# Optimization experiments

Measured on AMD Instinct MI355X. Metric: run time of the kernel, lower is better.

## Reference

```python
import jax, jax.numpy as jnp
import numpy as np

SPLINE_ORDER = 3
TOP_K = 2
NUM_EXPERTS = 8


def _gram_basis(x, beta_w):
    # x: (B, C, H, W) post-tanh. Returns (B, C*(S+1), H, W).
    P0 = jnp.ones_like(x)
    P1 = x
    ps = [P0, P1]
    for i in range(2, SPLINE_ORDER + 1):
        n, m = i - 1, i
        # beta(n, m) = (m+n)*(m-n)*n^2 / (m^2/(4n^2-1)) * beta_weights[n]
        beta = (m + n) * (m - n) * (n ** 2) * (4.0 * n ** 2 - 1.0) / (m ** 2) * beta_w[n]
        P2 = x * ps[-1] - beta * ps[-2]
        ps.append(P2)
    return jnp.concatenate(ps, axis=1)


def _expert(x, poly_w, beta_w):
    # tanh -> Gram polynomial basis -> SiLU -> conv2d (padding=1, stride=1)
    g = jax.nn.silu(_gram_basis(jnp.tanh(x), beta_w))
    return jax.lax.conv_general_dilated(
        g, poly_w[0], window_strides=(1, 1), padding=[(1, 1), (1, 1)],
        dimension_numbers=('NCHW', 'OIHW', 'NCHW'))


def _cv_squared(v):
    # torch.var is unbiased (ddof=1)
    return jnp.var(v, ddof=1) / (jnp.mean(v) ** 2 + 1e-10)


def reference(x, w_gate, poly_weights, beta_weights):
    B = x.shape[0]
    # gating input: global average pool -> (B, C)
    gate_x = jnp.mean(x, axis=(2, 3))
    probs = jax.nn.softmax(gate_x @ w_gate, axis=1)  # softmax BEFORE topk, as in source
    top_vals, top_idx = jax.lax.top_k(probs, TOP_K + 1)
    tk_vals = top_vals[:, :TOP_K]
    tk_idx = top_idx[:, :TOP_K]
    tk_gates = tk_vals / (jnp.sum(tk_vals, axis=1, keepdims=True) + 1e-6)
    gates = jnp.zeros_like(probs).at[jnp.arange(B)[:, None], tk_idx].set(tk_gates)
    importance = gates.sum(axis=0)
    load = jnp.sum(gates > 0, axis=0).astype(jnp.float32)  # eval-mode load
    loss = (_cv_squared(importance) + _cv_squared(load)) * 0.01
    # All experts share parameters (ModuleList([experts]*num_experts)), so
    # sum_e gates[b,e] * expert_e(x[b]) == gates.sum(1)[b] * expert(x[b]).
    y = _expert(x, poly_weights, beta_weights) * jnp.sum(gates, axis=1)[:, None, None, None]
    return y, loss


def setup_inputs() -> dict:
    key = jax.random.key(0)
    k1, k2, k3, k4 = jax.random.split(key, 4)
    x = jax.random.normal(k1, (16, 32, 192, 192), dtype=jnp.float32)
    w_gate = jax.random.normal(k2, (32, NUM_EXPERTS), dtype=jnp.float32) * 0.1
    poly_weights = jax.random.normal(k3, (1, 32, 32 * (SPLINE_ORDER + 1), 3, 3), dtype=jnp.float32) * 0.05
    beta_weights = jax.random.normal(k4, (SPLINE_ORDER + 1,), dtype=jnp.float32) * 0.01
    return {"x": x, "w_gate": w_gate, "poly_weights": poly_weights, "beta_weights": beta_weights}
```

## Files before the change

### kernel.cpp

```cpp
#include <hip/hip_runtime.h>

typedef unsigned short u16;
typedef unsigned int u32;
typedef __attribute__((ext_vector_type(8))) short bf16x8;
typedef __attribute__((ext_vector_type(4))) float f32x4;

static constexpr int B = 16, C = 32, H = 192, W = 192;
static constexpr int HW = H * W;
static constexpr int E = 8;
static constexpr int CO = 32;
static constexpr int NB = 96;
static constexpr long long NTOT = (long long)B * C * HW;
static constexpr float SILU1 = 0.7310585786300049f;

static constexpr size_t GP_OFF  = (size_t)NTOT * 2;
static constexpr size_t SCL_OFF = GP_OFF + (size_t)B * C * NB * 4;
static constexpr size_t SK_OFF  = SCL_OFF + 128;
static constexpr size_t SS_OFF  = SK_OFF + 288 * 4;
static constexpr size_t WF_OFF  = SS_OFF + 128;

__device__ inline u32 cvt_pk_bf16(float lo, float hi) {
    u32 r;
    asm("v_cvt_pk_bf16_f32 %0, %1, %2" : "=v"(r) : "v"(lo), "v"(hi));
    return r;
}
__device__ inline u16 f2b(float f) {
    u32 u = __float_as_uint(f);
    return (u16)((u + 0x7fffu + ((u >> 16) & 1u)) >> 16);
}
__device__ inline float silu_fast(float z) {
    return z * __builtin_amdgcn_rcpf(1.0f + __expf(-z));
}
__device__ inline float tanh_fast(float z) {
    float e = __expf(2.0f * z);
    return 1.0f - 2.0f * __builtin_amdgcn_rcpf(e + 1.0f);
}

__global__ __launch_bounds__(256) void stage1_prep(const float* __restrict__ x,
                                                   const float* __restrict__ pw,
                                                   u16* __restrict__ t_out,
                                                   float* __restrict__ gpart,
                                                   float* __restrict__ Sk,
                                                   float* __restrict__ Ssum,
                                                   u16* __restrict__ wfrag) {
    __shared__ float sg[2][4][16];
    __shared__ float sred[9][32][8];
    __shared__ float sks[288];
    const int blk = blockIdx.x, tid = threadIdx.x;
    if (blk < B * NB) {
        const int b = blk / NB, band = blk - (blk / NB) * NB;
        const int cp = tid & 15, part = tid >> 4;
        const size_t pbase = (size_t)b * HW + (size_t)(band * 2) * W;
        const float4* xa = (const float4*)(x + (size_t)(b * C + 2 * cp) * HW
                                             + (size_t)(band * 2) * W);
        const float4* xb = (const float4*)(x + (size_t)(b * C + 2 * cp + 1) * HW
                                             + (size_t)(band * 2) * W);
        u32* tw = (u32*)t_out;
        float s0 = 0.0f, s1 = 0.0f;
        #pragma unroll
        for (int k = 0; k < 6; ++k) {
            const int j = k * 16 + part;
            float4 a = xa[j], c = xb[j];
            s0 += (a.x + a.y) + (a.z + a.w);
            s1 += (c.x + c.y) + (c.z + c.w);
            u32 r0 = cvt_pk_bf16(tanh_fast(a.x), tanh_fast(c.x));
            u32 r1 = cvt_pk_bf16(tanh_fast(a.y), tanh_fast(c.y));
            u32 r2 = cvt_pk_bf16(tanh_fast(a.z), tanh_fast(c.z));
            u32 r3 = cvt_pk_bf16(tanh_fast(a.w), tanh_fast(c.w));
            u32* dst = tw + (pbase + (size_t)j * 4) * 16 + cp;
            dst[0] = r0; dst[16] = r1; dst[32] = r2; dst[48] = r3;
        }
        s0 += __shfl_down(s0, 32); s0 += __shfl_down(s0, 16);
        s1 += __shfl_down(s1, 32); s1 += __shfl_down(s1, 16);
        if ((part & 3) == 0) { sg[0][tid >> 6][cp] = s0; sg[1][tid >> 6][cp] = s1; }
        __syncthreads();
        if (tid < 32) {
            const int cpp = tid >> 1, o = tid & 1;
            gpart[(size_t)(b * C + tid) * NB + band] =
                (sg[o][0][cpp] + sg[o][1][cpp]) + (sg[o][2][cpp] + sg[o][3][cpp]);
        }
        return;
    }
    if (blk < B * NB + 108) {
        int j = (blk - B * NB) * 256 + tid;
        int e = j & 7, lane = (j >> 3) & 63, rest = j >> 9;
        int half = rest & 1, pt = rest >> 1;
        int p = pt / 9, tap = pt - p * 9;
        int co = half * 16 + (lane & 15);
        int ci = 32 + p * 32 + (lane >> 4) * 8 + e;
        wfrag[j] = f2b(pw[(size_t)co * 1152 + ci * 9 + tap]);
        return;
    }
    {
        const int co = tid & 31, sub = tid >> 5;
        #pragma unroll
        for (int k = 0; k < 9; ++k) {
            float s = 0.0f;
            #pragma unroll
            for (int i = 0; i < 4; ++i)
                s += pw[(size_t)co * 1152 + (sub * 4 + i) * 9 + k];
            sred[k][co][sub] = s;
        }
        __syncthreads();
        for (int j = tid; j < 288; j += 256) {
            int k = j >> 5, c = j & 31;
            float s = 0.0f;
            #pragma unroll
            for (int u = 0; u < 8; ++u) s += sred[k][c][u];
            sks[j] = s; Sk[j] = s;
        }
        __syncthreads();
        if (tid < 32) {
            float s = 0.0f;
            #pragma unroll
            for (int k = 0; k < 9; ++k) s += sks[k * 32 + tid];
            Ssum[tid] = s;
        }
    }
}

__global__ __launch_bounds__(512) void gate_k(const float* __restrict__ gpart,
                                              const float* __restrict__ wg,
                                              float* __restrict__ scl,
                                              float* __restrict__ out) {
    __shared__ float gx[B][C];
    __shared__ float lg[B][E];
    __shared__ float gt[B][E];
    const int tid = threadIdx.x;
    {
        const float4* gp = (const float4*)(gpart + (size_t)tid * NB);
        float s = 0.0f;
        #pragma unroll
        for (int k = 0; k < NB / 4; ++k) { float4 v = gp[k]; s += (v.x + v.y) + (v.z + v.w); }
        gx[tid >> 5][tid & 31] = s * (1.0f / HW);
    }
    __syncthreads();
    if (tid < B * E) {
        const int gb = tid >> 3, ge = tid & 7;
        float s = 0.0f;
        #pragma unroll
        for (int c = 0; c < C; ++c) s += gx[gb][c] * wg[c * E + ge];
        lg[gb][ge] = s;
    }
    __syncthreads();
    if (tid < B) {
        float p[E];
        float m = lg[tid][0];
        #pragma unroll
        for (int e = 1; e < E; ++e) m = fmaxf(m, lg[tid][e]);
        float sum = 0.0f;
        #pragma unroll
        for (int e = 0; e < E; ++e) { p[e] = __expf(lg[tid][e] - m); sum += p[e]; }
        float inv = 1.0f / sum;
        #pragma unroll
        for (int e = 0; e < E; ++e) p[e] *= inv;
        int i0 = 0; float v0g = p[0];
        #pragma unroll
        for (int e = 1; e < E; ++e) if (p[e] > v0g) { v0g = p[e]; i0 = e; }
        int i1 = -1; float v1g = -1.0f;
        #pragma unroll
        for (int e = 0; e < E; ++e) { if (e == i0) continue; if (p[e] > v1g) { v1g = p[e]; i1 = e; } }
        const float denom = v0g + v1g + 1e-6f;
        #pragma unroll
        for (int e = 0; e < E; ++e) gt[tid][e] = 0.0f;
        gt[tid][i0] = v0g / denom; gt[tid][i1] = v1g / denom;
        scl[tid] = gt[tid][i0] + gt[tid][i1];
    }
    __syncthreads();
    if (tid == 0) {
        float imp[E], ld[E];
        #pragma unroll
        for (int e = 0; e < E; ++e) { imp[e] = 0.0f; ld[e] = 0.0f; }
        for (int bb = 0; bb < B; ++bb)
            #pragma unroll
            for (int e = 0; e < E; ++e) {
                float g = gt[bb][e];
                imp[e] += g;
                if (g > 0.0f) ld[e] += 1.0f;
            }
        float mi = 0.0f, mld = 0.0f;
        #pragma unroll
        for (int e = 0; e < E; ++e) { mi += imp[e]; mld += ld[e]; }
        mi *= (1.0f / E); mld *= (1.0f / E);
        float vi = 0.0f, vl = 0.0f;
        #pragma unroll
        for (int e = 0; e < E; ++e) {
            float di = imp[e] - mi, dl = ld[e] - mld;
            vi += di * di; vl += dl * dl;
        }
        vi *= (1.0f / (E - 1)); vl *= (1.0f / (E - 1));
        out[NTOT] = (vi / (mi * mi + 1e-10f) + vl / (mld * mld + 1e-10f)) * 0.01f;
    }
}

static constexpr int GSTR = 40;

__global__ __launch_bounds__(256, 3) void conv_mfma(const u16* __restrict__ t_ws,
                                                 const u16* __restrict__ wfrag,
                                                 const float* __restrict__ beta_w,
                                                 const float* __restrict__ scl_ws,
                                                 const float* __restrict__ Sk,
                                                 const float* __restrict__ Ssum,
                                                 float* __restrict__ out) {
    __shared__ __align__(16) u16 gtile[2][324 * GSTR];

    const int b = blockIdx.z;
    const int gx0 = blockIdx.x << 4, gy0 = blockIdx.y << 4;
    const int tid = threadIdx.x;
    const int w = tid >> 6, lane = tid & 63, q = lane >> 4, ml = lane & 15;
    const float beta2 = 2.25f * beta_w[1];
    const float beta23 = beta2 + (300.0f / 9.0f) * beta_w[2];

    const int p0 = tid;
    int extra = -1;
    if ((tid & 3) == 0) extra = tid >> 2;
    else if ((tid & 63) == 1) extra = 64 + (tid >> 6);
    const int p1 = (extra >= 0) ? 256 + extra : -1;

    u32 pk0[16], pk1[16];
    bool v0, v1 = false;
    {
        int py = p0 / 18, px = p0 - py * 18;
        int gy = gy0 + py - 1, gx = gx0 + px - 1;
        v0 = (unsigned)gy < (unsigned)H && (unsigned)gx < (unsigned)W;
        if (v0) {
            const uint4* tp = (const uint4*)(t_ws + (((size_t)b * HW + (size_t)gy * W + gx) << 5));
            *(uint4*)&pk0[0]  = tp[0];
            *(uint4*)&pk0[4]  = tp[1];
            *(uint4*)&pk0[8]  = tp[2];
            *(uint4*)&pk0[12] = tp[3];
        } else {
            #pragma unroll
            for (int cc = 0; cc < 16; ++cc) pk0[cc] = 0u;
        }
        if (p1 >= 0) {
            int py1 = p1 / 18, px1 = p1 - py1 * 18;
            int gy1 = gy0 + py1 - 1, gx1 = gx0 + px1 - 1;
            v1 = (unsigned)gy1 < (unsigned)H && (unsigned)gx1 < (unsigned)W;
            if (v1) {
                const uint4* tp = (const uint4*)(t_ws + (((size_t)b * HW + (size_t)gy1 * W + gx1) << 5));
                *(uint4*)&pk1[0]  = tp[0];
                *(uint4*)&pk1[4]  = tp[1];
                *(uint4*)&pk1[8]  = tp[2];
                *(uint4*)&pk1[12] = tp[3];
            }
        }
        if (!v1) {
            #pragma unroll
            for (int cc = 0; cc < 16; ++cc) pk1[cc] = 0u;
        }
    }

    const float sc = scl_ws[b];

#define BQUAD(P, BUF, SLOT, QI)                                                 \
    do {                                                                        \
        if (!(SLOT) || p1 >= 0) {                                               \
            const bool vv = (SLOT) ? v1 : v0;                                   \
            const u32* pk = (SLOT) ? pk1 : pk0;                                 \
            const int pix = (SLOT) ? p1 : p0;                                   \
            u32 rq[4];                                                          \
            if (vv) {                                                           \
                _Pragma("unroll")                                               \
                for (int i = 0; i < 4; ++i) {                                   \
                    const int cc = (QI) * 4 + i;                                \
                    float tl = __uint_as_float(pk[cc] << 16);                   \
                    float th = __uint_as_float(pk[cc] & 0xffff0000u);           \
                    float ul, uh;                                               \
                    if ((P) == 0) { ul = tl; uh = th; }                         \
                    else if ((P) == 1) { ul = fmaf(tl, tl, -beta2); uh = fmaf(th, th, -beta2); } \
                    else { ul = tl * fmaf(tl, tl, -beta23); uh = th * fmaf(th, th, -beta23); } \
                    rq[i] = cvt_pk_bf16(silu_fast(ul), silu_fast(uh));          \
                }                                                               \
            } else { rq[0] = 0u; rq[1] = 0u; rq[2] = 0u; rq[3] = 0u; }          \
            *(uint4*)&gtile[BUF][pix * GSTR + (QI) * 8] = *(const uint4*)rq;    \
        }                                                                       \
    } while (0)

    f32x4 acc[4][2];
    #pragma unroll
    for (int a = 0; a < 4; ++a) {
        acc[a][0] = (f32x4){0.0f, 0.0f, 0.0f, 0.0f};
        acc[a][1] = (f32x4){0.0f, 0.0f, 0.0f, 0.0f};
    }

#define MFMA_DX(P, BUF, DX, ...)                                                \
    do {                                                                        \
        const u16* wf = wfrag + (size_t)(P) * 9216;                             \
        bf16x8 bfr[3][2];                                                       \
        _Pragma("unroll")                                                       \
        for (int dyi = 0; dyi < 3; ++dyi) {                                     \
            const int tap = dyi * 3 + (DX);                                     \
            bfr[dyi][0] = *(const bf16x8*)(wf + ((size_t)(tap * 2 + 0) * 64 + lane) * 8); \
            bfr[dyi][1] = *(const bf16x8*)(wf + ((size_t)(tap * 2 + 1) * 64 + lane) * 8); \
        }                                                                       \
        bf16x8 af6[6];                                                          \
        _Pragma("unroll")                                                       \
        for (int rl = 0; rl < 6; ++rl)                                          \
            af6[rl] = *(const bf16x8*)                                          \
                &gtile[BUF][(((w << 2) + rl) * 18 + ml + (DX)) * GSTR + (q << 3)]; \
        __VA_ARGS__;                                                            \
        _Pragma("unroll")                                                       \
        for (int rl = 0; rl < 6; ++rl) {                                        \
            _Pragma("unroll")                                                   \
            for (int dyi = 0; dyi < 3; ++dyi) {                                 \
                const int a = rl - dyi;                                         \
                if (a >= 0 && a < 4) {                                          \
                    acc[a][0] = __builtin_amdgcn_mfma_f32_16x16x32_bf16(af6[rl], bfr[dyi][0], acc[a][0], 0, 0, 0); \
                    acc[a][1] = __builtin_amdgcn_mfma_f32_16x16x32_bf16(af6[rl], bfr[dyi][1], acc[a][1], 0, 0, 0); \
                }                                                               \
            }                                                                   \
        }                                                                       \
    } while (0)

    BQUAD(0, 0, 0, 0); BQUAD(0, 0, 0, 1); BQUAD(0, 0, 0, 2); BQUAD(0, 0, 0, 3);
    BQUAD(0, 0, 1, 0); BQUAD(0, 0, 1, 1); BQUAD(0, 0, 1, 2); BQUAD(0, 0, 1, 3);
    __syncthreads();
    MFMA_DX(0, 0, 0, BQUAD(1, 1, 0, 0); BQUAD(1, 1, 0, 1); BQUAD(1, 1, 0, 2));
    MFMA_DX(0, 0, 1, BQUAD(1, 1, 0, 3); BQUAD(1, 1, 1, 0); BQUAD(1, 1, 1, 1));
    MFMA_DX(0, 0, 2, BQUAD(1, 1, 1, 2); BQUAD(1, 1, 1, 3));
    __syncthreads();
    MFMA_DX(1, 1, 0, BQUAD(2, 0, 0, 0); BQUAD(2, 0, 0, 1); BQUAD(2, 0, 0, 2));
    MFMA_DX(1, 1, 1, BQUAD(2, 0, 0, 3); BQUAD(2, 0, 1, 0); BQUAD(2, 0, 1, 1));
    MFMA_DX(1, 1, 2, BQUAD(2, 0, 1, 2); BQUAD(2, 0, 1, 3));
    __syncthreads();
    MFMA_DX(2, 0, 0, (void)0);
    MFMA_DX(2, 0, 1, (void)0);
    MFMA_DX(2, 0, 2, (void)0);

#undef BQUAD
#undef MFMA_DX

    const bool interior = (blockIdx.x > 0) && (blockIdx.x < 11) &&
                          (blockIdx.y > 0) && (blockIdx.y < 11);
    #pragma unroll
    for (int half = 0; half < 2; ++half) {
        const int co = half * 16 + ml;
        const float bfull = SILU1 * Ssum[co];
        #pragma unroll
        for (int a = 0; a < 4; ++a) {
            const int y = gy0 + (w << 2) + a;
            float ov[4];
            #pragma unroll
            for (int r = 0; r < 4; ++r) {
                float bias = bfull;
                if (!interior) {
                    const int xg = gx0 + (q << 2) + r;
                    bias = 0.0f;
                    #pragma unroll
                    for (int k = 0; k < 9; ++k) {
                        int yy = y + k / 3 - 1, xx = xg + k % 3 - 1;
                        if ((unsigned)yy < (unsigned)H && (unsigned)xx < (unsigned)W)
                            bias += Sk[k * 32 + co];
                    }
                    bias *= SILU1;
                }
                ov[r] = (acc[a][half][r] + bias) * sc;
            }
            *(float4*)&out[((size_t)(b * CO + co) * H + y) * W + gx0 + (q << 2)] = *(float4*)ov;
        }
    }
}

extern "C" void kernel_launch(void* const* d_in, const int* in_sizes, int n_in,
                              void* d_out, int out_size, void* d_ws, size_t ws_size,
                              hipStream_t stream) {
    const float* x  = (const float*)d_in[0];
    const float* wg = (const float*)d_in[1];
    const float* pw = (const float*)d_in[2];
    const float* bw = (const float*)d_in[3];
    float* out = (float*)d_out;
    char* ws = (char*)d_ws;
    u16*   t_ws  = (u16*)ws;
    float* gpart = (float*)(ws + GP_OFF);
    float* scl   = (float*)(ws + SCL_OFF);
    float* Sk    = (float*)(ws + SK_OFF);
    float* Ssum  = (float*)(ws + SS_OFF);
    u16*   wfrag = (u16*)(ws + WF_OFF);

    stage1_prep<<<dim3(B * NB + 109), 256, 0, stream>>>(x, pw, t_ws, gpart, Sk, Ssum, wfrag);
    gate_k<<<dim3(1), 512, 0, stream>>>(gpart, wg, scl, out);
    conv_mfma<<<dim3(12, 12, B), 256, 0, stream>>>(t_ws, wfrag, bw, scl, Sk, Ssum, out);
}
```

Before: 242.2 us.

## Single-buffer conv LDS tile and raise occupancy target to six blocks

Replaces the double-buffered shared-memory basis tile with a single buffer, so basis computation and MFMA phases now run serially with extra barriers between them. Launch bounds rise from 3 to 6 blocks per CU, which halves LDS use per block and pushes the compiler to cut register use. The bet is that more resident waves hide latency better than the explicit in-block overlap did. The cost is lost intra-block overlap, two extra barriers, and possible register spills under the tighter budget.

```diff
diff --git a/kernel.cpp b/kernel.cpp
--- a/kernel.cpp
+++ b/kernel.cpp
@@ -195,14 +195,14 @@
 
 static constexpr int GSTR = 40;
 
-__global__ __launch_bounds__(256, 3) void conv_mfma(const u16* __restrict__ t_ws,
+__global__ __launch_bounds__(256, 6) void conv_mfma(const u16* __restrict__ t_ws,
                                                  const u16* __restrict__ wfrag,
                                                  const float* __restrict__ beta_w,
                                                  const float* __restrict__ scl_ws,
                                                  const float* __restrict__ Sk,
                                                  const float* __restrict__ Ssum,
                                                  float* __restrict__ out) {
-    __shared__ __align__(16) u16 gtile[2][324 * GSTR];
+    __shared__ __align__(16) u16 gtile[324 * GSTR];
 
     const int b = blockIdx.z;
     const int gx0 = blockIdx.x << 4, gy0 = blockIdx.y << 4;
@@ -253,27 +253,35 @@
 
     const float sc = scl_ws[b];
 
-#define BQUAD(P, BUF, SLOT, QI)                                                 \
+#define BASIS(P)                                                                \
     do {                                                                        \
-        if (!(SLOT) || p1 >= 0) {                                               \
-            const bool vv = (SLOT) ? v1 : v0;                                   \
-            const u32* pk = (SLOT) ? pk1 : pk0;                                 \
-            const int pix = (SLOT) ? p1 : p0;                                   \
-            u32 rq[4];                                                          \
+        _Pragma("unroll")                                                       \
+        for (int slot = 0; slot < 2; ++slot) {                                  \
+            const int pix = slot ? p1 : p0;                                     \
+            if (slot && p1 < 0) continue;                                       \
+            const bool vv = slot ? v1 : v0;                                     \
+            const u32* pk = slot ? pk1 : pk0;                                   \
+            u32 r[16];                                                          \
             if (vv) {                                                           \
                 _Pragma("unroll")                                               \
-                for (int i = 0; i < 4; ++i) {                                   \
-                    const int cc = (QI) * 4 + i;                                \
+                for (int cc = 0; cc < 16; ++cc) {                               \
                     float tl = __uint_as_float(pk[cc] << 16);                   \
                     float th = __uint_as_float(pk[cc] & 0xffff0000u);           \
                     float ul, uh;                                               \
                     if ((P) == 0) { ul = tl; uh = th; }                         \
                     else if ((P) == 1) { ul = fmaf(tl, tl, -beta2); uh = fmaf(th, th, -beta2); } \
                     else { ul = tl * fmaf(tl, tl, -beta23); uh = th * fmaf(th, th, -beta23); } \
-                    rq[i] = cvt_pk_bf16(silu_fast(ul), silu_fast(uh));          \
+                    r[cc] = cvt_pk_bf16(silu_fast(ul), silu_fast(uh));          \
                 }                                                               \
-            } else { rq[0] = 0u; rq[1] = 0u; rq[2] = 0u; rq[3] = 0u; }          \
-            *(uint4*)&gtile[BUF][pix * GSTR + (QI) * 8] = *(const uint4*)rq;    \
+            } else {                                                            \
+                _Pragma("unroll")                                               \
+                for (int cc = 0; cc < 16; ++cc) r[cc] = 0u;                     \
+            }                                                                   \
+            uint4* dst = (uint4*)&gtile[pix * GSTR];                            \
+            dst[0] = *(const uint4*)&r[0];                                      \
+            dst[1] = *(const uint4*)&r[4];                                      \
+            dst[2] = *(const uint4*)&r[8];                                      \
+            dst[3] = *(const uint4*)&r[12];                                     \
         }                                                                       \
     } while (0)
 
@@ -284,7 +292,7 @@
         acc[a][1] = (f32x4){0.0f, 0.0f, 0.0f, 0.0f};
     }
 
-#define MFMA_DX(P, BUF, DX, ...)                                                \
+#define MFMA_DX(P, DX)                                                          \
     do {                                                                        \
         const u16* wf = wfrag + (size_t)(P) * 9216;                             \
         bf16x8 bfr[3][2];                                                       \
@@ -298,8 +306,7 @@
         _Pragma("unroll")                                                       \
         for (int rl = 0; rl < 6; ++rl)                                          \
             af6[rl] = *(const bf16x8*)                                          \
-                &gtile[BUF][(((w << 2) + rl) * 18 + ml + (DX)) * GSTR + (q << 3)]; \
-        __VA_ARGS__;                                                            \
+                &gtile[(((w << 2) + rl) * 18 + ml + (DX)) * GSTR + (q << 3)];   \
         _Pragma("unroll")                                                       \
         for (int rl = 0; rl < 6; ++rl) {                                        \
             _Pragma("unroll")                                                   \
@@ -313,22 +320,19 @@
         }                                                                       \
     } while (0)
 
-    BQUAD(0, 0, 0, 0); BQUAD(0, 0, 0, 1); BQUAD(0, 0, 0, 2); BQUAD(0, 0, 0, 3);
-    BQUAD(0, 0, 1, 0); BQUAD(0, 0, 1, 1); BQUAD(0, 0, 1, 2); BQUAD(0, 0, 1, 3);
-    __syncthreads();
-    MFMA_DX(0, 0, 0, BQUAD(1, 1, 0, 0); BQUAD(1, 1, 0, 1); BQUAD(1, 1, 0, 2));
-    MFMA_DX(0, 0, 1, BQUAD(1, 1, 0, 3); BQUAD(1, 1, 1, 0); BQUAD(1, 1, 1, 1));
-    MFMA_DX(0, 0, 2, BQUAD(1, 1, 1, 2); BQUAD(1, 1, 1, 3));
-    __syncthreads();
-    MFMA_DX(1, 1, 0, BQUAD(2, 0, 0, 0); BQUAD(2, 0, 0, 1); BQUAD(2, 0, 0, 2));
-    MFMA_DX(1, 1, 1, BQUAD(2, 0, 0, 3); BQUAD(2, 0, 1, 0); BQUAD(2, 0, 1, 1));
-    MFMA_DX(1, 1, 2, BQUAD(2, 0, 1, 2); BQUAD(2, 0, 1, 3));
-    __syncthreads();
-    MFMA_DX(2, 0, 0, (void)0);
-    MFMA_DX(2, 0, 1, (void)0);
-    MFMA_DX(2, 0, 2, (void)0);
-
-#undef BQUAD
+    BASIS(0);
+    __syncthreads();
+    MFMA_DX(0, 0); MFMA_DX(0, 1); MFMA_DX(0, 2);
+    __syncthreads();
+    BASIS(1);
+    __syncthreads();
+    MFMA_DX(1, 0); MFMA_DX(1, 1); MFMA_DX(1, 2);
+    __syncthreads();
+    BASIS(2);
+    __syncthreads();
+    MFMA_DX(2, 0); MFMA_DX(2, 1); MFMA_DX(2, 2);
+
+#undef BASIS
 #undef MFMA_DX
 
     const bool interior = (blockIdx.x > 0) && (blockIdx.x < 11) &&
```

Measured after the change: 311.8 us. 28.7% more time.
